# Kernel optimization log

Hardware: AMD Instinct MI355X
Metric: run time of the kernel (lower is better)

The kernel has to match this reference:

```python
import jax, jax.numpy as jnp
import numpy as np

# Dims
B_, L_, IN_ = 16, 8192, 57
DM, DS, HD, EXP, NL, OUT = 64, 32, 32, 2, 2, 6
DI = EXP * DM            # 128 inner dim
NH = DI // HD            # 4 heads
DPROJ = 2 * DI + 2 * DS + NH  # z, x, B, C, dt


def setup_inputs() -> dict:
    key = jax.random.key(0)
    ks = jax.random.split(key, 8)
    def rn(k, shape, scale=0.02):
        return jax.random.normal(k, shape, dtype=jnp.float32) * scale
    return {
        "x": jax.random.normal(ks[0], (B_, L_, IN_), dtype=jnp.float32),
        "W_in": rn(ks[1], (IN_, DM)),
        "b_in": jnp.zeros((DM,), jnp.float32),
        "in_proj_W": rn(ks[2], (NL, DM, DPROJ)),
        "in_proj_b": jnp.zeros((NL, DPROJ), jnp.float32),
        "A_log": jnp.log(jnp.broadcast_to(jnp.arange(1, NH + 1, dtype=jnp.float32), (NL, NH))),
        "D": jnp.ones((NL, NH), jnp.float32),
        "dt_bias": rn(ks[3], (NL, NH), 0.1),
        "out_proj_W": rn(ks[4], (NL, DI, DM)),
        "out_proj_b": jnp.zeros((NL, DM), jnp.float32),
        "cls_W": rn(ks[5], (DM, OUT)),
        "cls_b": jnp.zeros((OUT,), jnp.float32),
    }


def _mamba_layer(x, W, b, A_log, D, dt_bias, Wo, bo):
    """SISO Mamba3-style selective scan block. x: [B, L, DM]."""
    Bsz, L, _ = x.shape
    zxbcdt = x @ W + b                               # [B, L, DPROJ]
    z, xin, Bm, Cm, dt = jnp.split(
        zxbcdt, [DI, 2 * DI, 2 * DI + DS, 2 * DI + 2 * DS], axis=-1)
    dt = jax.nn.softplus(dt + dt_bias)               # [B, L, NH]
    A = -jnp.exp(A_log)                              # [NH], per-head scalar (SISO)
    xin = jax.nn.silu(xin).reshape(Bsz, L, NH, HD)   # [B, L, NH, HD]
    Bm = jax.nn.silu(Bm)                             # [B, L, DS]
    Cm = jax.nn.silu(Cm)                             # [B, L, DS]
    decay = jnp.exp(dt * A)                          # [B, L, NH]

    def step(h, inp):
        # h: [B, NH, HD, DS]
        xt, bt, ct, dtt, dect = inp
        h = dect[:, :, None, None] * h + (dtt[:, :, None] * xt)[..., None] * bt[:, None, None, :]
        yt = jnp.einsum('bhpn,bn->bhp', h, ct)       # [B, NH, HD]
        return h, yt

    h0 = jnp.zeros((Bsz, NH, HD, DS), x.dtype)
    xs = (jnp.moveaxis(xin, 1, 0), jnp.moveaxis(Bm, 1, 0), jnp.moveaxis(Cm, 1, 0),
          jnp.moveaxis(dt, 1, 0), jnp.moveaxis(decay, 1, 0))
    _, ys = jax.lax.scan(step, h0, xs)               # [L, B, NH, HD]
    y = jnp.moveaxis(ys, 0, 1) + D[None, None, :, None] * xin
    y = y.reshape(Bsz, L, DI) * jax.nn.silu(z)       # gated output
    return y @ Wo + bo                               # [B, L, DM]


def reference(x, W_in, b_in, in_proj_W, in_proj_b, A_log, D, dt_bias,
              out_proj_W, out_proj_b, cls_W, cls_b):
    h = x @ W_in + b_in                              # linear_in
    for l in range(NL):                              # residual Mamba stack
        h = h + _mamba_layer(h, in_proj_W[l], in_proj_b[l], A_log[l], D[l],
                             dt_bias[l], out_proj_W[l], out_proj_b[l])
    pooled = h.mean(axis=1)                          # AdaptiveAvgPool1d(1)
    return pooled @ cls_W + cls_b                    # classifier [B, OUT]
```

## Files before the change

kernel.cpp:

```cpp
#include <hip/hip_runtime.h>

#define BSZ   16
#define LSEQ  8192
#define DMDL  64
#define DSD   32
#define HDD   32
#define NHD   4
#define DIN   128
#define NLAY  2
#define NOUTC 6
#define DPRJ  324
#define QC    64
#define NCH   128
#define NT21  21

typedef __attribute__((ext_vector_type(8))) short bf16x8;
typedef __attribute__((ext_vector_type(4))) float f32x4;

__device__ float          g_h0[BSZ*LSEQ*DMDL];
__device__ unsigned short g_xy[BSZ*LSEQ*DIN];
__device__ unsigned short g_Ba[BSZ*LSEQ*DSD];
__device__ unsigned short g_Ca[BSZ*LSEQ*DSD];
__device__ float          g_dt[BSZ*LSEQ*NHD];
__device__ float          g_pc[BSZ*LSEQ*NHD];
__device__ float          g_cS[BSZ*NCH*NHD*HDD*DSD];
__device__ unsigned short g_Hb[BSZ*NCH*NHD*HDD*DSD];
__device__ float          g_cL[BSZ*NCH*NHD];
__device__ float          g_ppc[BSZ*NCH*DMDL];
__device__ unsigned short g_wf[NLAY*NT21*2*64*8];
__device__ unsigned short g_wo[NLAY*4*4*64*8];

__device__ __forceinline__ float silu_f(float v){ return v / (1.0f + __expf(-v)); }
__device__ __forceinline__ float softplus_f(float v){ return (v > 15.0f) ? v : __logf(1.0f + __expf(v)); }
__device__ __forceinline__ unsigned short f2bf(float f){
  union { float f; unsigned u; } v; v.f = f;
  unsigned r = v.u + 0x7FFFu + ((v.u >> 16) & 1u);
  return (unsigned short)(r >> 16);
}
__device__ __forceinline__ float bf2f(unsigned short h){
  union { unsigned u; float f; } v; v.u = ((unsigned)h) << 16;
  return v.f;
}

#define LSTR 132
__global__ __launch_bounds__(256) void k_linin(
    const float* __restrict__ x, const float* __restrict__ W,
    const float* __restrict__ bias)
{
  __shared__ float xt[57*LSTR];
  __shared__ float wl[57*64];
  const int tid = threadIdx.x;
  const long tb = (long)blockIdx.x * 128;
  for (int i = tid; i < 912; i += 256)
    *(float4*)&wl[i*4] = *(const float4*)&W[i*4];
  for (int i = tid; i < 1824; i += 256){
    float4 v = *(const float4*)&x[tb*57 + (long)i*4];
    const int e = i*4;
    int t0 = e / 57;
    int k0 = e - t0*57;
    float vv[4] = {v.x, v.y, v.z, v.w};
    #pragma unroll
    for (int j = 0; j < 4; ++j){
      int t = t0, k = k0 + j;
      if (k >= 57){ t += 1; k -= 57; }
      xt[k*LSTR + t] = vv[j];
    }
  }
  __syncthreads();
  const int d0 = (tid & 7) * 8;
  const int t0 = (tid >> 3) * 4;
  float acc[4][8];
  #pragma unroll
  for (int i = 0; i < 4; ++i)
    #pragma unroll
    for (int j = 0; j < 8; ++j) acc[i][j] = 0.f;
  #pragma unroll 4
  for (int k = 0; k < 57; ++k){
    float4 xv4 = *(const float4*)&xt[k*LSTR + t0];
    float4 w0  = *(const float4*)&wl[k*64 + d0];
    float4 w1  = *(const float4*)&wl[k*64 + d0 + 4];
    float xv[4] = {xv4.x, xv4.y, xv4.z, xv4.w};
    float wv[8] = {w0.x, w0.y, w0.z, w0.w, w1.x, w1.y, w1.z, w1.w};
    #pragma unroll
    for (int i = 0; i < 4; ++i)
      #pragma unroll
      for (int j = 0; j < 8; ++j) acc[i][j] += xv[i] * wv[j];
  }
  float4 bb0 = *(const float4*)&bias[d0];
  float4 bb1 = *(const float4*)&bias[d0 + 4];
  #pragma unroll
  for (int i = 0; i < 4; ++i){
    float4 o0, o1;
    o0.x = acc[i][0] + bb0.x; o0.y = acc[i][1] + bb0.y;
    o0.z = acc[i][2] + bb0.z; o0.w = acc[i][3] + bb0.w;
    o1.x = acc[i][4] + bb1.x; o1.y = acc[i][5] + bb1.y;
    o1.z = acc[i][6] + bb1.z; o1.w = acc[i][7] + bb1.w;
    *(float4*)&g_h0[(tb + t0 + i)*64 + d0]     = o0;
    *(float4*)&g_h0[(tb + t0 + i)*64 + d0 + 4] = o1;
  }
}

__global__ __launch_bounds__(128) void k_wprep(const float* __restrict__ W)
{
  const int nt = blockIdx.x;
  const int l  = blockIdx.y;
  const int ks = threadIdx.x >> 6, lane = threadIdx.x & 63;
  const float* Wl = W + (long)l*64*DPRJ;
  const int n  = nt*16 + (lane & 15);
  const int k0 = ks*32 + (lane >> 4)*8;
  unsigned short v[8];
  #pragma unroll
  for (int j = 0; j < 8; ++j)
    v[j] = (n < DPRJ) ? f2bf(Wl[(k0 + j)*DPRJ + n]) : (unsigned short)0;
  unsigned short* d = &g_wf[((((long)l*NT21 + nt)*2 + ks)*64 + lane)*8];
  *(ushort4*)&d[0] = make_ushort4(v[0], v[1], v[2], v[3]);
  *(ushort4*)&d[4] = make_ushort4(v[4], v[5], v[6], v[7]);
}

__global__ __launch_bounds__(64) void k_wprep2(const float* __restrict__ Wo)
{
  const int nt = blockIdx.x >> 2, ks = blockIdx.x & 3, l = blockIdx.y;
  const int lane = threadIdx.x;
  const int n  = nt*16 + (lane & 15);
  const int k0 = ks*32 + (lane >> 4)*8;
  const float* Wl = Wo + (long)l*128*64;
  unsigned short* d = &g_wo[((((long)l*4 + nt)*4 + ks)*64 + lane)*8];
  unsigned short v[8];
  #pragma unroll
  for (int j = 0; j < 8; ++j) v[j] = f2bf(Wl[(k0 + j)*64 + n]);
  *(ushort4*)&d[0] = make_ushort4(v[0], v[1], v[2], v[3]);
  *(ushort4*)&d[4] = make_ushort4(v[4], v[5], v[6], v[7]);
}

#define OP 136
__global__ __launch_bounds__(256) void k_proj(
    const float* __restrict__ bias, const float* __restrict__ dt_bias, int l)
{
  __shared__ __align__(16) unsigned short Afr[8*2*64*8];
  __shared__ __align__(16) unsigned short Obuf[128*OP];
  const int tid = threadIdx.x;
  const long tb = (long)blockIdx.x * 128;
  #pragma unroll
  for (int r = 0; r < 4; ++r){
    const int c = tid + 256*r;
    const int t = c >> 3, k8 = c & 7;
    float4 f0 = *(const float4*)&g_h0[(tb + t)*64 + k8*8];
    float4 f1 = *(const float4*)&g_h0[(tb + t)*64 + k8*8 + 4];
    const int mt = t >> 4, ks = k8 >> 2, q = k8 & 3, ln = (t & 15) + 16*q;
    unsigned short* d = &Afr[(((mt*2 + ks)*64) + ln)*8];
    *(ushort4*)&d[0] = make_ushort4(f2bf(f0.x), f2bf(f0.y), f2bf(f0.z), f2bf(f0.w));
    *(ushort4*)&d[4] = make_ushort4(f2bf(f1.x), f2bf(f1.y), f2bf(f1.z), f2bf(f1.w));
  }
  __syncthreads();
  const int w = tid >> 6, lane = tid & 63;
  const int colq = lane & 15, rowq = lane >> 4;
  bf16x8 a[2][2];
  #pragma unroll
  for (int m = 0; m < 2; ++m)
    #pragma unroll
    for (int ks = 0; ks < 2; ++ks)
      a[m][ks] = *(const bf16x8*)&Afr[((((2*w + m)*2 + ks)*64) + lane)*8];
  const float* bl = bias + (long)l*DPRJ;
  const unsigned short* wf = &g_wf[(long)l*NT21*2*64*8];
  #pragma unroll
  for (int nti = 0; nti < 8; ++nti){
    const int nt = 8 + nti;
    bf16x8 b0 = *(const bf16x8*)&wf[((nt*2 + 0)*64 + lane)*8];
    bf16x8 b1 = *(const bf16x8*)&wf[((nt*2 + 1)*64 + lane)*8];
    const float b = bl[nt*16 + colq];
    #pragma unroll
    for (int m = 0; m < 2; ++m){
      f32x4 acc = {0.f, 0.f, 0.f, 0.f};
      acc = __builtin_amdgcn_mfma_f32_16x16x32_bf16(a[m][0], b0, acc, 0, 0, 0);
      acc = __builtin_amdgcn_mfma_f32_16x16x32_bf16(a[m][1], b1, acc, 0, 0, 0);
      const int tbase = (2*w + m)*16 + rowq*4;
      const int ocol = nti*16 + colq;
      #pragma unroll
      for (int r = 0; r < 4; ++r)
        Obuf[(tbase + r)*OP + ocol] = f2bf(silu_f(acc[r] + b));
    }
  }
  __syncthreads();
  #pragma unroll
  for (int it = 0; it < 8; ++it){
    const int i = tid + 256*it;
    const int t = i >> 4, c0 = (i & 15) * 8;
    *(uint4*)&g_xy[(tb + t)*128 + c0] = *(const uint4*)&Obuf[t*OP + c0];
  }
  __syncthreads();
  #pragma unroll
  for (int nti = 0; nti < 4; ++nti){
    const int nt = 16 + nti;
    bf16x8 b0 = *(const bf16x8*)&wf[((nt*2 + 0)*64 + lane)*8];
    bf16x8 b1 = *(const bf16x8*)&wf[((nt*2 + 1)*64 + lane)*8];
    const float b = bl[nt*16 + colq];
    #pragma unroll
    for (int m = 0; m < 2; ++m){
      f32x4 acc = {0.f, 0.f, 0.f, 0.f};
      acc = __builtin_amdgcn_mfma_f32_16x16x32_bf16(a[m][0], b0, acc, 0, 0, 0);
      acc = __builtin_amdgcn_mfma_f32_16x16x32_bf16(a[m][1], b1, acc, 0, 0, 0);
      const int tbase = (2*w + m)*16 + rowq*4;
      const int ocol = nti*16 + colq;
      #pragma unroll
      for (int r = 0; r < 4; ++r)
        Obuf[(tbase + r)*OP + ocol] = f2bf(silu_f(acc[r] + b));
    }
  }
  {
    bf16x8 b0 = *(const bf16x8*)&wf[((20*2 + 0)*64 + lane)*8];
    bf16x8 b1 = *(const bf16x8*)&wf[((20*2 + 1)*64 + lane)*8];
    #pragma unroll
    for (int m = 0; m < 2; ++m){
      f32x4 acc = {0.f, 0.f, 0.f, 0.f};
      acc = __builtin_amdgcn_mfma_f32_16x16x32_bf16(a[m][0], b0, acc, 0, 0, 0);
      acc = __builtin_amdgcn_mfma_f32_16x16x32_bf16(a[m][1], b1, acc, 0, 0, 0);
      if (colq < 4){
        const int tbase = (2*w + m)*16 + rowq*4;
        const float b = bl[320 + colq] + dt_bias[l*4 + colq];
        #pragma unroll
        for (int r = 0; r < 4; ++r)
          g_dt[(tb + tbase + r)*4 + colq] = softplus_f(acc[r] + b);
      }
    }
  }
  __syncthreads();
  #pragma unroll
  for (int it = 0; it < 4; ++it){
    const int i = tid + 256*it;
    const int t = i >> 3, k = i & 7;
    const int c0 = (k & 3) * 8;
    if (k < 4){
      *(uint4*)&g_Ba[(tb + t)*32 + c0] = *(const uint4*)&Obuf[t*OP + c0];
    } else {
      *(uint4*)&g_Ca[(tb + t)*32 + c0] = *(const uint4*)&Obuf[t*OP + 32 + c0];
    }
  }
}

#define SB 40
#define ST 72
__device__ __forceinline__ int xsw(int p, int s){
  return p*ST + (((((s) >> 3) + ((p) >> 2)) & 7) << 3) + ((s) & 7);
}
__device__ __forceinline__ int xsw8(int p, int blk){
  return p*ST + (((((blk)) + ((p) >> 2)) & 7) << 3);
}
__global__ __launch_bounds__(256) void k_s1(
    const float* __restrict__ A_log, const float* __restrict__ Dp, int l)
{
  __shared__ __align__(16) unsigned short u_bc[2*64*SB];
  __shared__ __align__(16) unsigned short Bbt[32*ST];
  __shared__ __align__(16) unsigned short Mb[2*64*ST];
  __shared__ float Sl[4*64];
  __shared__ float dts[4*64];
  __shared__ float wls[4*64];
  const int tid = threadIdx.x;
  const int cI = blockIdx.x, b = blockIdx.y;
  const long tb = (long)b*LSEQ + (long)cI*QC;
  unsigned short* Bb = u_bc;
  unsigned short* Cb = u_bc + 64*SB;
  const int s0 = tid >> 3, p40 = (tid & 7) * 4;
  for (int i = tid; i < 512; i += 256){
    const int s = i >> 3, n0 = (i & 7) * 4;
    ushort4 bu = *(const ushort4*)&g_Ba[(tb + s)*32 + n0];
    ushort4 cu = *(const ushort4*)&g_Ca[(tb + s)*32 + n0];
    *(ushort4*)&Bb[s*SB + n0] = bu;
    *(ushort4*)&Cb[s*SB + n0] = cu;
    Bbt[xsw(n0    , s)] = bu.x;
    Bbt[xsw(n0 + 1, s)] = bu.y;
    Bbt[xsw(n0 + 2, s)] = bu.z;
    Bbt[xsw(n0 + 3, s)] = bu.w;
  }
  {
    const int h = tid >> 6, t = tid & 63;
    const float Ah = -__expf(A_log[l*4 + h]);
    const float v = g_dt[(tb + t)*4 + h];
    float x = v * Ah;
    #pragma unroll
    for (int d = 1; d < 64; d <<= 1){
      float y = __shfl_up(x, d);
      if (t >= d) x += y;
    }
    Sl[h*64 + t] = x;
    dts[h*64 + t] = v;
    const float send = __shfl(x, 63);
    wls[h*64 + t] = __expf(send - x) * v;
    if (t == 63) g_cL[((long)b*NCH + cI)*4 + h] = x;
    g_pc[(tb + t)*4 + h] = __expf(x);
  }
  ushort4 xr0 = *(const ushort4*)&g_xy[(tb + s0)*128 + p40];
  ushort4 xr1 = *(const ushort4*)&g_xy[(tb + s0 + 32)*128 + p40];
  __syncthreads();
  const int w = tid >> 6, lane = tid & 63;
  const int colq = lane & 15, rowq = lane >> 4;
  float Greg[3][4];
  int Gmt[3], Gst[3];
  #pragma unroll
  for (int rep = 0; rep < 3; ++rep){
    const int k = w + rep*4;
    if (k < 10){
      const int mt = (k >= 6) ? 3 : ((k >= 3) ? 2 : ((k >= 1) ? 1 : 0));
      const int st = k - mt*(mt+1)/2;
      Gmt[rep] = mt; Gst[rep] = st;
      bf16x8 af = *(const bf16x8*)&Cb[(mt*16 + colq)*SB + rowq*8];
      bf16x8 bf = *(const bf16x8*)&Bb[(st*16 + colq)*SB + rowq*8];
      f32x4 acc = {0.f, 0.f, 0.f, 0.f};
      acc = __builtin_amdgcn_mfma_f32_16x16x32_bf16(af, bf, acc, 0, 0, 0);
      #pragma unroll
      for (int r = 0; r < 4; ++r) Greg[rep][r] = acc[r];
    } else { Gmt[rep] = -1; Gst[rep] = 0; }
  }
  #pragma unroll
  for (int rep = 0; rep < 2; ++rep){
    const int k = w + rep*4;
    if (k < 6){
      const int mt = (k < 3) ? 0 : ((k < 5) ? 1 : 2);
      const int st = (k < 3) ? (k + 1) : ((k < 5) ? (k - 1) : 3);
      #pragma unroll
      for (int r = 0; r < 4; ++r){
        const int t = mt*16 + rowq*4 + r, s = st*16 + colq;
        Mb[xsw(t, s)] = 0;
        Mb[64*ST + xsw(t, s)] = 0;
      }
    }
  }
  __syncthreads();
  unsigned short* Xt0 = u_bc;
  unsigned short* Xt1 = u_bc + 32*ST;
  for (int h = 0; h < NHD; ++h){
    unsigned short* Xt  = (h & 1) ? Xt1 : Xt0;
    unsigned short* Mbh = Mb + (h & 1)*64*ST;
    Xt[xsw(p40    , s0)] = xr0.x;
    Xt[xsw(p40 + 1, s0)] = xr0.y;
    Xt[xsw(p40 + 2, s0)] = xr0.z;
    Xt[xsw(p40 + 3, s0)] = xr0.w;
    Xt[xsw(p40    , s0 + 32)] = xr1.x;
    Xt[xsw(p40 + 1, s0 + 32)] = xr1.y;
    Xt[xsw(p40 + 2, s0 + 32)] = xr1.z;
    Xt[xsw(p40 + 3, s0 + 32)] = xr1.w;
    #pragma unroll
    for (int rep = 0; rep < 3; ++rep){
      if (Gmt[rep] >= 0){
        const int mt = Gmt[rep], st = Gst[rep];
        const int s = st*16 + colq;
        const float sls = Sl[h*64 + s];
        const float dv = dts[h*64 + s];
        #pragma unroll
        for (int r = 0; r < 4; ++r){
          const int t = mt*16 + rowq*4 + r;
          const float m = (s <= t) ? __expf(Sl[h*64 + t] - sls) * dv * Greg[rep][r] : 0.f;
          Mbh[xsw(t, s)] = f2bf(m);
        }
      }
    }
    __syncthreads();
    if (h < 3){
      xr0 = *(const ushort4*)&g_xy[(tb + s0)*128 + (h + 1)*32 + p40];
      xr1 = *(const ushort4*)&g_xy[(tb + s0 + 32)*128 + (h + 1)*32 + p40];
    }
    const float Dh = Dp[l*4 + h];
    bf16x8 a0 = *(const bf16x8*)&Mbh[xsw8(w*16 + colq, rowq)];
    bf16x8 a1 = *(const bf16x8*)&Mbh[xsw8(w*16 + colq, rowq + 4)];
    bf16x8 xb0, xb1;
    #pragma unroll
    for (int nt = 0; nt < 2; ++nt){
      bf16x8 b0 = *(const bf16x8*)&Xt[xsw8(nt*16 + colq, rowq)];
      bf16x8 b1 = *(const bf16x8*)&Xt[xsw8(nt*16 + colq, rowq + 4)];
      if (nt == (w & 1)){ xb0 = b0; xb1 = b1; }
      f32x4 acc = {0.f, 0.f, 0.f, 0.f};
      acc = __builtin_amdgcn_mfma_f32_16x16x32_bf16(a0, b0, acc, 0, 0, 0);
      acc = __builtin_amdgcn_mfma_f32_16x16x32_bf16(a1, b1, acc, 0, 0, 0);
      const int p = nt*16 + colq;
      #pragma unroll
      for (int r = 0; r < 4; ++r){
        const int t = w*16 + rowq*4 + r;
        const float xv = bf2f(Xt[xsw(p, t)]);
        g_xy[(tb + t)*128 + h*32 + p] = f2bf(acc[r] + Dh*xv);
      }
    }
    {
      union { bf16x8 v; unsigned short u[8]; } sx0, sx1, sa0, sa1;
      sx0.v = xb0; sx1.v = xb1;
      #pragma unroll
      for (int j = 0; j < 8; ++j){
        sa0.u[j] = f2bf(bf2f(sx0.u[j]) * wls[h*64 + rowq*8 + j]);
        sa1.u[j] = f2bf(bf2f(sx1.u[j]) * wls[h*64 + 32 + rowq*8 + j]);
      }
      const int mt = w & 1, nt2 = w >> 1;
      bf16x8 bb0 = *(const bf16x8*)&Bbt[xsw8(nt2*16 + colq, rowq)];
      bf16x8 bb1 = *(const bf16x8*)&Bbt[xsw8(nt2*16 + colq, rowq + 4)];
      f32x4 acc = {0.f, 0.f, 0.f, 0.f};
      acc = __builtin_amdgcn_mfma_f32_16x16x32_bf16(sa0.v, bb0, acc, 0, 0, 0);
      acc = __builtin_amdgcn_mfma_f32_16x16x32_bf16(sa1.v, bb1, acc, 0, 0, 0);
      const long base = (((long)b*NCH + cI)*NHD + h)*(HDD*DSD);
      const int n = nt2*16 + colq;
      #pragma unroll
      for (int r = 0; r < 4; ++r){
        const int p = mt*16 + rowq*4 + r;
        g_cS[base + p*32 + n] = acc[r];
      }
    }
  }
}

__global__ __launch_bounds__(128) void k_s2()
{
  const int h = blockIdx.x >> 3, seg = blockIdx.x & 7, b = blockIdx.y;
  const int idx = seg*128 + threadIdx.x;
  float H = 0.f;
  for (int c = 0; c < NCH; ++c){
    const long o = (((long)b*NCH + c)*NHD + h)*1024 + idx;
    const float cs = g_cS[o];
    const float lg = g_cL[((long)b*NCH + c)*4 + h];
    g_Hb[o] = f2bf(H);
    H = __expf(lg) * H + cs;
  }
}

__global__ __launch_bounds__(256) void k_s3(
    const float* __restrict__ ipb, const float* __restrict__ bo, int l, int finalLayer)
{
  __shared__ __align__(16) unsigned short Hb[128*40];
  __shared__ __align__(16) unsigned short Cb[64*40];
  __shared__ __align__(16) unsigned short gl[64*136];
  __shared__ float pcl[4*64];
  __shared__ float csum[4*64];
  const int tid = threadIdx.x;
  const int cI = blockIdx.x, b = blockIdx.y;
  const long tb = (long)b*LSEQ + (long)cI*QC;
  const long hbase = (((long)b*NCH + cI)*NHD)*(long)(HDD*DSD);
  for (int i = tid; i < 512; i += 256){
    const int hp = i >> 2, n0 = (i & 3) * 8;
    *(uint4*)&Hb[hp*40 + n0] = *(const uint4*)&g_Hb[hbase + hp*32 + n0];
  }
  for (int i = tid; i < 512; i += 256){
    const int t = i >> 3, n0 = (i & 7) * 4;
    *(ushort4*)&Cb[t*40 + n0] = *(const ushort4*)&g_Ca[(tb + t)*32 + n0];
  }
  { int t = tid >> 2, h = tid & 3; pcl[h*64 + t] = g_pc[(tb + t)*4 + h]; }
  __syncthreads();
  const int w = tid >> 6, lane = tid & 63;
  const int colq = lane & 15, rowq = lane >> 4;
  const float* blz = ipb + (long)l*DPRJ;
  const unsigned short* wfz = &g_wf[(long)l*NT21*2*64*8];
  {
    const long tok0 = tb + w*16 + colq;
    bf16x8 h0a, h0b;
    {
      float4 f0 = *(const float4*)&g_h0[tok0*64 + rowq*8];
      float4 f1 = *(const float4*)&g_h0[tok0*64 + rowq*8 + 4];
      float4 f2 = *(const float4*)&g_h0[tok0*64 + 32 + rowq*8];
      float4 f3 = *(const float4*)&g_h0[tok0*64 + 32 + rowq*8 + 4];
      union { bf16x8 v; unsigned short u[8]; } ca, cb2;
      ca.u[0]=f2bf(f0.x); ca.u[1]=f2bf(f0.y); ca.u[2]=f2bf(f0.z); ca.u[3]=f2bf(f0.w);
      ca.u[4]=f2bf(f1.x); ca.u[5]=f2bf(f1.y); ca.u[6]=f2bf(f1.z); ca.u[7]=f2bf(f1.w);
      cb2.u[0]=f2bf(f2.x); cb2.u[1]=f2bf(f2.y); cb2.u[2]=f2bf(f2.z); cb2.u[3]=f2bf(f2.w);
      cb2.u[4]=f2bf(f3.x); cb2.u[5]=f2bf(f3.y); cb2.u[6]=f2bf(f3.z); cb2.u[7]=f2bf(f3.w);
      h0a = ca.v; h0b = cb2.v;
    }
    bf16x8 a = *(const bf16x8*)&Cb[(w*16 + colq)*40 + rowq*8];
    #pragma unroll
    for (int nt = 0; nt < 8; ++nt){
      bf16x8 bfr = *(const bf16x8*)&Hb[(nt*16 + colq)*40 + rowq*8];
      f32x4 acc = {0.f, 0.f, 0.f, 0.f};
      acc = __builtin_amdgcn_mfma_f32_16x16x32_bf16(a, bfr, acc, 0, 0, 0);
      bf16x8 bz0 = *(const bf16x8*)&wfz[((nt*2 + 0)*64 + lane)*8];
      bf16x8 bz1 = *(const bf16x8*)&wfz[((nt*2 + 1)*64 + lane)*8];
      f32x4 zac = {0.f, 0.f, 0.f, 0.f};
      zac = __builtin_amdgcn_mfma_f32_16x16x32_bf16(h0a, bz0, zac, 0, 0, 0);
      zac = __builtin_amdgcn_mfma_f32_16x16x32_bf16(h0b, bz1, zac, 0, 0, 0);
      const int hp = nt*16 + colq;
      const int h = hp >> 5;
      const float zb = blz[hp];
      #pragma unroll
      for (int r = 0; r < 4; ++r){
        const int t = w*16 + rowq*4 + r;
        const long tok = tb + t;
        const float v = pcl[h*64 + t] * acc[r] + bf2f(g_xy[tok*128 + hp]);
        gl[t*136 + hp] = f2bf(v * silu_f(zac[r] + zb));
      }
    }
  }
  __syncthreads();
  const unsigned short* wo = &g_wo[(long)l*4*4*512];
  #pragma unroll
  for (int nt2 = 0; nt2 < 4; ++nt2){
    f32x4 acc = {0.f, 0.f, 0.f, 0.f};
    #pragma unroll
    for (int ks = 0; ks < 4; ++ks){
      bf16x8 a = *(const bf16x8*)&gl[(w*16 + colq)*136 + ks*32 + rowq*8];
      bf16x8 bfr = *(const bf16x8*)&wo[(nt2*4 + ks)*512 + lane*8];
      acc = __builtin_amdgcn_mfma_f32_16x16x32_bf16(a, bfr, acc, 0, 0, 0);
    }
    const int dm = nt2*16 + colq;
    const float bb = bo[l*64 + dm];
    float part = 0.f;
    #pragma unroll
    for (int r = 0; r < 4; ++r){
      const int t = w*16 + rowq*4 + r;
      const long tok = tb + t;
      const float o = acc[r] + bb + g_h0[tok*64 + dm];
      g_h0[tok*64 + dm] = o;
      part += o;
    }
    if (finalLayer){
      part += __shfl_xor(part, 16);
      part += __shfl_xor(part, 32);
      if (rowq == 0) csum[w*64 + dm] = part;
    }
  }
  if (finalLayer){
    __syncthreads();
    if (tid < 64){
      g_ppc[((long)b*NCH + cI)*64 + tid] =
        csum[tid] + csum[64 + tid] + csum[128 + tid] + csum[192 + tid];
    }
  }
}

__global__ __launch_bounds__(64) void k_pool2(
    const float* __restrict__ cW, const float* __restrict__ cb,
    float* __restrict__ out)
{
  __shared__ float pl[64];
  const int b = blockIdx.x, tid = threadIdx.x;
  float s = 0.f;
  for (int c = 0; c < NCH; ++c) s += g_ppc[((long)b*NCH + c)*64 + tid];
  pl[tid] = s * (1.0f / 8192.0f);
  __syncthreads();
  if (tid < NOUTC){
    float acc = cb[tid];
    for (int dm = 0; dm < 64; ++dm) acc += pl[dm] * cW[dm*NOUTC + tid];
    out[b*NOUTC + tid] = acc;
  }
}

extern "C" void kernel_launch(void* const* d_in, const int* in_sizes, int n_in,
                              void* d_out, int out_size, void* d_ws, size_t ws_size,
                              hipStream_t stream)
{
  const float* x      = (const float*)d_in[0];
  const float* W_in   = (const float*)d_in[1];
  const float* b_in   = (const float*)d_in[2];
  const float* ipW    = (const float*)d_in[3];
  const float* ipb    = (const float*)d_in[4];
  const float* A_log  = (const float*)d_in[5];
  const float* Dp     = (const float*)d_in[6];
  const float* dtb    = (const float*)d_in[7];
  const float* opW    = (const float*)d_in[8];
  const float* opb    = (const float*)d_in[9];
  const float* clsW   = (const float*)d_in[10];
  const float* clsb   = (const float*)d_in[11];
  float* out = (float*)d_out;
  (void)d_ws; (void)ws_size;

  k_wprep<<<dim3(NT21, NLAY), 128, 0, stream>>>(ipW);
  k_wprep2<<<dim3(16, NLAY), 64, 0, stream>>>(opW);
  k_linin<<<1024, 256, 0, stream>>>(x, W_in, b_in);
  for (int l = 0; l < NLAY; ++l){
    k_proj<<<1024, 256, 0, stream>>>(ipb, dtb, l);
    k_s1<<<dim3(NCH, BSZ), 256, 0, stream>>>(A_log, Dp, l);
    k_s2<<<dim3(32, BSZ), 128, 0, stream>>>();
    k_s3<<<dim3(NCH, BSZ), 256, 0, stream>>>(ipb, opb, l, (l == NLAY-1) ? 1 : 0);
  }
  k_pool2<<<BSZ, 64, 0, stream>>>(clsW, clsb, out);
}
```

Measured before the change: 340.6 us.

## Fuse input projection into chunk-scan stage one kernel

Merges the projection kernel into the first chunked-scan kernel. Each 64-token chunk block now computes B, C, dt and per-head x projections with MFMA directly into shared memory, instead of writing B, dt and x to global memory and reading them back. This removes one launch and a large global round trip. The cost is extra per-head barriers and single-buffered Mb/Xt, which serializes heads that were previously overlapped through double buffering. C is still written out for the later stage.

```diff
diff --git a/kernel.cpp b/kernel.cpp
--- a/kernel.cpp
+++ b/kernel.cpp
@@ -19,9 +19,7 @@
 
 __device__ float          g_h0[BSZ*LSEQ*DMDL];
 __device__ unsigned short g_xy[BSZ*LSEQ*DIN];
-__device__ unsigned short g_Ba[BSZ*LSEQ*DSD];
 __device__ unsigned short g_Ca[BSZ*LSEQ*DSD];
-__device__ float          g_dt[BSZ*LSEQ*NHD];
 __device__ float          g_pc[BSZ*LSEQ*NHD];
 __device__ float          g_cS[BSZ*NCH*NHD*HDD*DSD];
 __device__ unsigned short g_Hb[BSZ*NCH*NHD*HDD*DSD];
@@ -132,18 +130,33 @@
   *(ushort4*)&d[4] = make_ushort4(v[4], v[5], v[6], v[7]);
 }
 
-#define OP 136
-__global__ __launch_bounds__(256) void k_proj(
-    const float* __restrict__ bias, const float* __restrict__ dt_bias, int l)
-{
-  __shared__ __align__(16) unsigned short Afr[8*2*64*8];
-  __shared__ __align__(16) unsigned short Obuf[128*OP];
+#define SB 40
+#define ST 72
+__device__ __forceinline__ int xsw(int p, int s){
+  return p*ST + (((((s) >> 3) + ((p) >> 2)) & 7) << 3) + ((s) & 7);
+}
+__device__ __forceinline__ int xsw8(int p, int blk){
+  return p*ST + (((((blk)) + ((p) >> 2)) & 7) << 3);
+}
+__global__ __launch_bounds__(256) void k_ps(
+    const float* __restrict__ ipb, const float* __restrict__ dtb,
+    const float* __restrict__ A_log, const float* __restrict__ Dp, int l)
+{
+  __shared__ __align__(16) unsigned short Afr[4*2*64*8];
+  __shared__ __align__(16) unsigned short Bb[64*SB];
+  __shared__ __align__(16) unsigned short Cb[64*SB];
+  __shared__ __align__(16) unsigned short Bbt[32*ST];
+  __shared__ __align__(16) unsigned short Xt[32*ST];
+  __shared__ __align__(16) unsigned short Mb[64*ST];
+  __shared__ float Sl[4*64];
+  __shared__ float dts[4*64];
+  __shared__ float wls[4*64];
+  __shared__ float dtl[64*4];
   const int tid = threadIdx.x;
-  const long tb = (long)blockIdx.x * 128;
-  #pragma unroll
-  for (int r = 0; r < 4; ++r){
-    const int c = tid + 256*r;
-    const int t = c >> 3, k8 = c & 7;
+  const int cI = blockIdx.x, b = blockIdx.y;
+  const long tb = (long)b*LSEQ + (long)cI*QC;
+  for (int i = tid; i < 512; i += 256){
+    const int t = i >> 3, k8 = i & 7;
     float4 f0 = *(const float4*)&g_h0[(tb + t)*64 + k8*8];
     float4 f1 = *(const float4*)&g_h0[(tb + t)*64 + k8*8 + 4];
     const int mt = t >> 4, ks = k8 >> 2, q = k8 & 3, ln = (t & 15) + 16*q;
@@ -154,127 +167,54 @@
   __syncthreads();
   const int w = tid >> 6, lane = tid & 63;
   const int colq = lane & 15, rowq = lane >> 4;
-  bf16x8 a[2][2];
-  #pragma unroll
-  for (int m = 0; m < 2; ++m)
-    #pragma unroll
-    for (int ks = 0; ks < 2; ++ks)
-      a[m][ks] = *(const bf16x8*)&Afr[((((2*w + m)*2 + ks)*64) + lane)*8];
-  const float* bl = bias + (long)l*DPRJ;
+  const float* bl = ipb + (long)l*DPRJ;
   const unsigned short* wf = &g_wf[(long)l*NT21*2*64*8];
-  #pragma unroll
-  for (int nti = 0; nti < 8; ++nti){
-    const int nt = 8 + nti;
-    bf16x8 b0 = *(const bf16x8*)&wf[((nt*2 + 0)*64 + lane)*8];
-    bf16x8 b1 = *(const bf16x8*)&wf[((nt*2 + 1)*64 + lane)*8];
-    const float b = bl[nt*16 + colq];
-    #pragma unroll
-    for (int m = 0; m < 2; ++m){
-      f32x4 acc = {0.f, 0.f, 0.f, 0.f};
-      acc = __builtin_amdgcn_mfma_f32_16x16x32_bf16(a[m][0], b0, acc, 0, 0, 0);
-      acc = __builtin_amdgcn_mfma_f32_16x16x32_bf16(a[m][1], b1, acc, 0, 0, 0);
-      const int tbase = (2*w + m)*16 + rowq*4;
-      const int ocol = nti*16 + colq;
-      #pragma unroll
-      for (int r = 0; r < 4; ++r)
-        Obuf[(tbase + r)*OP + ocol] = f2bf(silu_f(acc[r] + b));
-    }
-  }
-  __syncthreads();
-  #pragma unroll
-  for (int it = 0; it < 8; ++it){
-    const int i = tid + 256*it;
-    const int t = i >> 4, c0 = (i & 15) * 8;
-    *(uint4*)&g_xy[(tb + t)*128 + c0] = *(const uint4*)&Obuf[t*OP + c0];
-  }
-  __syncthreads();
+  const bf16x8 a0 = *(const bf16x8*)&Afr[((w*2 + 0)*64 + lane)*8];
+  const bf16x8 a1 = *(const bf16x8*)&Afr[((w*2 + 1)*64 + lane)*8];
   #pragma unroll
   for (int nti = 0; nti < 4; ++nti){
     const int nt = 16 + nti;
     bf16x8 b0 = *(const bf16x8*)&wf[((nt*2 + 0)*64 + lane)*8];
     bf16x8 b1 = *(const bf16x8*)&wf[((nt*2 + 1)*64 + lane)*8];
-    const float b = bl[nt*16 + colq];
-    #pragma unroll
-    for (int m = 0; m < 2; ++m){
-      f32x4 acc = {0.f, 0.f, 0.f, 0.f};
-      acc = __builtin_amdgcn_mfma_f32_16x16x32_bf16(a[m][0], b0, acc, 0, 0, 0);
-      acc = __builtin_amdgcn_mfma_f32_16x16x32_bf16(a[m][1], b1, acc, 0, 0, 0);
-      const int tbase = (2*w + m)*16 + rowq*4;
-      const int ocol = nti*16 + colq;
+    const float bia = bl[nt*16 + colq];
+    f32x4 acc = {0.f, 0.f, 0.f, 0.f};
+    acc = __builtin_amdgcn_mfma_f32_16x16x32_bf16(a0, b0, acc, 0, 0, 0);
+    acc = __builtin_amdgcn_mfma_f32_16x16x32_bf16(a1, b1, acc, 0, 0, 0);
+    const int t4 = w*16 + rowq*4;
+    if (nti < 2){
+      const int n = nti*16 + colq;
+      #pragma unroll
+      for (int r = 0; r < 4; ++r){
+        const unsigned short v = f2bf(silu_f(acc[r] + bia));
+        Bb[(t4 + r)*SB + n] = v;
+        Bbt[xsw(n, t4 + r)] = v;
+      }
+    } else {
+      const int n = (nti - 2)*16 + colq;
       #pragma unroll
       for (int r = 0; r < 4; ++r)
-        Obuf[(tbase + r)*OP + ocol] = f2bf(silu_f(acc[r] + b));
+        Cb[(t4 + r)*SB + n] = f2bf(silu_f(acc[r] + bia));
     }
   }
   {
     bf16x8 b0 = *(const bf16x8*)&wf[((20*2 + 0)*64 + lane)*8];
     bf16x8 b1 = *(const bf16x8*)&wf[((20*2 + 1)*64 + lane)*8];
-    #pragma unroll
-    for (int m = 0; m < 2; ++m){
-      f32x4 acc = {0.f, 0.f, 0.f, 0.f};
-      acc = __builtin_amdgcn_mfma_f32_16x16x32_bf16(a[m][0], b0, acc, 0, 0, 0);
-      acc = __builtin_amdgcn_mfma_f32_16x16x32_bf16(a[m][1], b1, acc, 0, 0, 0);
-      if (colq < 4){
-        const int tbase = (2*w + m)*16 + rowq*4;
-        const float b = bl[320 + colq] + dt_bias[l*4 + colq];
-        #pragma unroll
-        for (int r = 0; r < 4; ++r)
-          g_dt[(tb + tbase + r)*4 + colq] = softplus_f(acc[r] + b);
-      }
-    }
-  }
-  __syncthreads();
-  #pragma unroll
-  for (int it = 0; it < 4; ++it){
-    const int i = tid + 256*it;
-    const int t = i >> 3, k = i & 7;
-    const int c0 = (k & 3) * 8;
-    if (k < 4){
-      *(uint4*)&g_Ba[(tb + t)*32 + c0] = *(const uint4*)&Obuf[t*OP + c0];
-    } else {
-      *(uint4*)&g_Ca[(tb + t)*32 + c0] = *(const uint4*)&Obuf[t*OP + 32 + c0];
-    }
-  }
-}
-
-#define SB 40
-#define ST 72
-__device__ __forceinline__ int xsw(int p, int s){
-  return p*ST + (((((s) >> 3) + ((p) >> 2)) & 7) << 3) + ((s) & 7);
-}
-__device__ __forceinline__ int xsw8(int p, int blk){
-  return p*ST + (((((blk)) + ((p) >> 2)) & 7) << 3);
-}
-__global__ __launch_bounds__(256) void k_s1(
-    const float* __restrict__ A_log, const float* __restrict__ Dp, int l)
-{
-  __shared__ __align__(16) unsigned short u_bc[2*64*SB];
-  __shared__ __align__(16) unsigned short Bbt[32*ST];
-  __shared__ __align__(16) unsigned short Mb[2*64*ST];
-  __shared__ float Sl[4*64];
-  __shared__ float dts[4*64];
-  __shared__ float wls[4*64];
-  const int tid = threadIdx.x;
-  const int cI = blockIdx.x, b = blockIdx.y;
-  const long tb = (long)b*LSEQ + (long)cI*QC;
-  unsigned short* Bb = u_bc;
-  unsigned short* Cb = u_bc + 64*SB;
-  const int s0 = tid >> 3, p40 = (tid & 7) * 4;
-  for (int i = tid; i < 512; i += 256){
-    const int s = i >> 3, n0 = (i & 7) * 4;
-    ushort4 bu = *(const ushort4*)&g_Ba[(tb + s)*32 + n0];
-    ushort4 cu = *(const ushort4*)&g_Ca[(tb + s)*32 + n0];
-    *(ushort4*)&Bb[s*SB + n0] = bu;
-    *(ushort4*)&Cb[s*SB + n0] = cu;
-    Bbt[xsw(n0    , s)] = bu.x;
-    Bbt[xsw(n0 + 1, s)] = bu.y;
-    Bbt[xsw(n0 + 2, s)] = bu.z;
-    Bbt[xsw(n0 + 3, s)] = bu.w;
-  }
+    f32x4 acc = {0.f, 0.f, 0.f, 0.f};
+    acc = __builtin_amdgcn_mfma_f32_16x16x32_bf16(a0, b0, acc, 0, 0, 0);
+    acc = __builtin_amdgcn_mfma_f32_16x16x32_bf16(a1, b1, acc, 0, 0, 0);
+    if (colq < 4){
+      const float bia = bl[320 + colq] + dtb[l*4 + colq];
+      const int t4 = w*16 + rowq*4;
+      #pragma unroll
+      for (int r = 0; r < 4; ++r)
+        dtl[(t4 + r)*4 + colq] = softplus_f(acc[r] + bia);
+    }
+  }
+  __syncthreads();
   {
-    const int h = tid >> 6, t = tid & 63;
+    const int h = w, t = lane;
     const float Ah = -__expf(A_log[l*4 + h]);
-    const float v = g_dt[(tb + t)*4 + h];
+    const float v = dtl[t*4 + h];
     float x = v * Ah;
     #pragma unroll
     for (int d = 1; d < 64; d <<= 1){
@@ -288,11 +228,10 @@
     if (t == 63) g_cL[((long)b*NCH + cI)*4 + h] = x;
     g_pc[(tb + t)*4 + h] = __expf(x);
   }
-  ushort4 xr0 = *(const ushort4*)&g_xy[(tb + s0)*128 + p40];
-  ushort4 xr1 = *(const ushort4*)&g_xy[(tb + s0 + 32)*128 + p40];
-  __syncthreads();
-  const int w = tid >> 6, lane = tid & 63;
-  const int colq = lane & 15, rowq = lane >> 4;
+  {
+    const int t = tid >> 2, c0 = (tid & 3) * 8;
+    *(uint4*)&g_Ca[(tb + t)*32 + c0] = *(const uint4*)&Cb[t*SB + c0];
+  }
   float Greg[3][4];
   int Gmt[3], Gst[3];
   #pragma unroll
@@ -320,24 +259,26 @@
       for (int r = 0; r < 4; ++r){
         const int t = mt*16 + rowq*4 + r, s = st*16 + colq;
         Mb[xsw(t, s)] = 0;
-        Mb[64*ST + xsw(t, s)] = 0;
-      }
-    }
-  }
-  __syncthreads();
-  unsigned short* Xt0 = u_bc;
-  unsigned short* Xt1 = u_bc + 32*ST;
+      }
+    }
+  }
+  __syncthreads();
   for (int h = 0; h < NHD; ++h){
-    unsigned short* Xt  = (h & 1) ? Xt1 : Xt0;
-    unsigned short* Mbh = Mb + (h & 1)*64*ST;
-    Xt[xsw(p40    , s0)] = xr0.x;
-    Xt[xsw(p40 + 1, s0)] = xr0.y;
-    Xt[xsw(p40 + 2, s0)] = xr0.z;
-    Xt[xsw(p40 + 3, s0)] = xr0.w;
-    Xt[xsw(p40    , s0 + 32)] = xr1.x;
-    Xt[xsw(p40 + 1, s0 + 32)] = xr1.y;
-    Xt[xsw(p40 + 2, s0 + 32)] = xr1.z;
-    Xt[xsw(p40 + 3, s0 + 32)] = xr1.w;
+    #pragma unroll
+    for (int half = 0; half < 2; ++half){
+      const int nt = 8 + 2*h + half;
+      bf16x8 b0 = *(const bf16x8*)&wf[((nt*2 + 0)*64 + lane)*8];
+      bf16x8 b1 = *(const bf16x8*)&wf[((nt*2 + 1)*64 + lane)*8];
+      const float bia = bl[nt*16 + colq];
+      f32x4 acc = {0.f, 0.f, 0.f, 0.f};
+      acc = __builtin_amdgcn_mfma_f32_16x16x32_bf16(a0, b0, acc, 0, 0, 0);
+      acc = __builtin_amdgcn_mfma_f32_16x16x32_bf16(a1, b1, acc, 0, 0, 0);
+      const int p = half*16 + colq;
+      const int t4 = w*16 + rowq*4;
+      #pragma unroll
+      for (int r = 0; r < 4; ++r)
+        Xt[xsw(p, t4 + r)] = f2bf(silu_f(acc[r] + bia));
+    }
     #pragma unroll
     for (int rep = 0; rep < 3; ++rep){
       if (Gmt[rep] >= 0){
@@ -349,18 +290,14 @@
         for (int r = 0; r < 4; ++r){
           const int t = mt*16 + rowq*4 + r;
           const float m = (s <= t) ? __expf(Sl[h*64 + t] - sls) * dv * Greg[rep][r] : 0.f;
-          Mbh[xsw(t, s)] = f2bf(m);
+          Mb[xsw(t, s)] = f2bf(m);
         }
       }
     }
     __syncthreads();
-    if (h < 3){
-      xr0 = *(const ushort4*)&g_xy[(tb + s0)*128 + (h + 1)*32 + p40];
-      xr1 = *(const ushort4*)&g_xy[(tb + s0 + 32)*128 + (h + 1)*32 + p40];
-    }
     const float Dh = Dp[l*4 + h];
-    bf16x8 a0 = *(const bf16x8*)&Mbh[xsw8(w*16 + colq, rowq)];
-    bf16x8 a1 = *(const bf16x8*)&Mbh[xsw8(w*16 + colq, rowq + 4)];
+    bf16x8 ma0 = *(const bf16x8*)&Mb[xsw8(w*16 + colq, rowq)];
+    bf16x8 ma1 = *(const bf16x8*)&Mb[xsw8(w*16 + colq, rowq + 4)];
     bf16x8 xb0, xb1;
     #pragma unroll
     for (int nt = 0; nt < 2; ++nt){
@@ -368,8 +305,8 @@
       bf16x8 b1 = *(const bf16x8*)&Xt[xsw8(nt*16 + colq, rowq + 4)];
       if (nt == (w & 1)){ xb0 = b0; xb1 = b1; }
       f32x4 acc = {0.f, 0.f, 0.f, 0.f};
-      acc = __builtin_amdgcn_mfma_f32_16x16x32_bf16(a0, b0, acc, 0, 0, 0);
-      acc = __builtin_amdgcn_mfma_f32_16x16x32_bf16(a1, b1, acc, 0, 0, 0);
+      acc = __builtin_amdgcn_mfma_f32_16x16x32_bf16(ma0, b0, acc, 0, 0, 0);
+      acc = __builtin_amdgcn_mfma_f32_16x16x32_bf16(ma1, b1, acc, 0, 0, 0);
       const int p = nt*16 + colq;
       #pragma unroll
       for (int r = 0; r < 4; ++r){
@@ -400,6 +337,7 @@
         g_cS[base + p*32 + n] = acc[r];
       }
     }
+    __syncthreads();
   }
 }
 
@@ -558,8 +496,7 @@
   k_wprep2<<<dim3(16, NLAY), 64, 0, stream>>>(opW);
   k_linin<<<1024, 256, 0, stream>>>(x, W_in, b_in);
   for (int l = 0; l < NLAY; ++l){
-    k_proj<<<1024, 256, 0, stream>>>(ipb, dtb, l);
-    k_s1<<<dim3(NCH, BSZ), 256, 0, stream>>>(A_log, Dp, l);
+    k_ps<<<dim3(NCH, BSZ), 256, 0, stream>>>(ipb, dtb, A_log, Dp, l);
     k_s2<<<dim3(32, BSZ), 128, 0, stream>>>();
     k_s3<<<dim3(NCH, BSZ), 256, 0, stream>>>(ipb, opb, l, (l == NLAY-1) ? 1 : 0);
   }
```

Result: faster. 319.9 us (-6.1%).
